# Kernel optimization log

Hardware: AMD Instinct MI355X
Metric: run time of the kernel (lower is better)

## Reference

```python
import jax, jax.numpy as jnp
import numpy as np

B, C, N, T = 16, 32, 400, 12
R, G, E, H = 64, 16, 64, 2
DH = E // H
FE = 4 * E
N1 = N2 = N3 = N4 = 0.5


def layernorm(x, w, b, eps=1e-5):
    m = x.mean(-1, keepdims=True)
    v = x.var(-1, keepdims=True)
    return (x - m) / jnp.sqrt(v + eps) * w + b


def asym_adj(A):
    rowsum = A.sum(1)
    d_inv = jnp.where(rowsum > 0, 1.0 / rowsum, 0.0)
    return d_inv[:, None] * A


def gcn(x, supports, W, b):
    # CHGCNGCN with order=1: concat [x, x@a for a in supports] on channel dim, 1x1 conv
    outs = [x] + [jnp.einsum('bcvt,vw->bcwt', x, a) for a in supports]
    h = jnp.concatenate(outs, axis=1)
    return jnp.einsum('oc,bcvt->bovt', W, h) + b[None, :, None, None]


def setup_inputs() -> dict:
    key0 = jax.random.key(0)
    ks = jax.random.split(key0, 40)
    rn = lambda i, sh, s=1.0: jax.random.normal(ks[i], sh, dtype=jnp.float32) * s
    ru = lambda i, sh, s=1.0: jax.random.uniform(ks[i], sh, dtype=jnp.float32) * s
    inp = {
        'value': rn(0, (B, C, N, T)),
        'key': rn(1, (B, C, N, T)),
        'query': rn(2, (B, C, N, T)),
        'supports0': ru(3, (N, N), 1.0 / N),
        'supports1': ru(4, (N, N), 1.0 / N),
        'supports_r0': ru(5, (R, R), 1.0 / R),
        'supports_r1': ru(6, (R, R), 1.0 / R),
        'Mrg': ru(7, (R, G), 1.0 / R),
        'Mor': ru(8, (N, R), 1.0 / N),
        'D_S': ru(9, (N, N)),
        'W_conv1': rn(10, (E, C), (1.0 / C) ** 0.5),
        'b_conv1': jnp.zeros((E,), jnp.float32),
        'W_conv11': rn(11, (C, E), (1.0 / E) ** 0.5),
        'b_conv11': jnp.zeros((C,), jnp.float32),
        'W_gcn': rn(12, (C, 3 * C), (1.0 / (3 * C)) ** 0.5),
        'b_gcn': jnp.zeros((C,), jnp.float32),
        'W_embed': rn(13, (E, N), (1.0 / N) ** 0.5),
        'b_embed': jnp.zeros((E,), jnp.float32),
        'Wq': rn(14, (DH, DH), (1.0 / DH) ** 0.5),
        'Wk': rn(15, (DH, DH), (1.0 / DH) ** 0.5),
        'Wv': rn(16, (DH, DH), (1.0 / DH) ** 0.5),
        'W_fc': rn(17, (E, E), (1.0 / E) ** 0.5),
        'b_fc': jnp.zeros((E,), jnp.float32),
        'ln1_w': jnp.ones((E,), jnp.float32),
        'ln1_b': jnp.zeros((E,), jnp.float32),
        'ln2_w': jnp.ones((E,), jnp.float32),
        'ln2_b': jnp.zeros((E,), jnp.float32),
        'W_ff1': rn(18, (FE, E), (1.0 / E) ** 0.5),
        'b_ff1': jnp.zeros((FE,), jnp.float32),
        'W_ff2': rn(19, (E, FE), (1.0 / FE) ** 0.5),
        'b_ff2': jnp.zeros((E,), jnp.float32),
        'W_fs': rn(20, (E, E), (1.0 / E) ** 0.5),
        'b_fs': jnp.zeros((E,), jnp.float32),
        'W_fg': rn(21, (E, E), (1.0 / E) ** 0.5),
        'b_fg': jnp.zeros((E,), jnp.float32),
    }
    return inp


def _chgcn(x, supports, supports_r, Mrg, Mor, W_gcn, b_gcn):
    ho = gcn(x, supports, W_gcn, b_gcn)
    x_r = jnp.einsum('nr,bcnt->bcrt', Mor, x)            # Mor.T @ x
    hr = gcn(x_r, supports_r, W_gcn, b_gcn)
    xs = jnp.einsum('rg,bcrt->bcgt', Mrg, x_r)           # Mrg.T @ (Mor.T @ x)
    # data-dependent global adjacency (detached in torch -> stop_gradient)
    xg_mat = jnp.transpose(xs, (2, 1, 0, 3)).reshape(G, -1)   # (G, C*B*T)
    xgt_mat = jnp.transpose(xs, (3, 0, 1, 2)).reshape(-1, G)  # (T*B*C, G)
    Ag = jax.lax.stop_gradient(jax.nn.relu(xg_mat @ xgt_mat - 0.5))
    sg = [jax.nn.softmax(asym_adj(Ag), axis=-1),
          jax.nn.softmax(asym_adj(Ag.T), axis=-1)]
    xg = gcn(xs, sg, W_gcn, b_gcn)
    hr = hr + N1 * jax.nn.relu(jnp.einsum('rg,bcgt->bcrt', Mrg, xg))
    ho = ho + N2 * jax.nn.relu(jnp.einsum('nr,bcrt->bcnt', Mor, hr))
    hr = hr + N3 * jax.nn.relu(jnp.einsum('nr,bcnt->bcrt', Mor, ho))
    xg = xg + N4 * jax.nn.relu(jnp.einsum('rg,bcrt->bcgt', Mrg, hr))
    return ho, hr, xg


def _attention(q, Wq, Wk, Wv, W_fc, b_fc):
    # q: (B, N, T, E); value=key=query in STransformer.forward
    qh = q.reshape(B, N, T, H, DH)
    qq = jnp.einsum('bnthd,ed->bnthe', qh, Wq)
    kk = jnp.einsum('bnthd,ed->bnthe', qh, Wk)
    vv = jnp.einsum('bnthd,ed->bnthe', qh, Wv)
    energy = jnp.einsum('bqthd,bkthd->bqkth', qq, kk)
    attn = jax.nn.softmax(energy / (E ** 0.5), axis=2)
    out = jnp.einsum('bqkth,bkthd->bqthd', attn, vv).reshape(B, N, T, E)
    return jnp.einsum('bnte,oe->bnto', out, W_fc) + b_fc


def reference(value, key, query, supports0, supports1, supports_r0, supports_r1,
              Mrg, Mor, D_S, W_conv1, b_conv1, W_conv11, b_conv11, W_gcn, b_gcn,
              W_embed, b_embed, Wq, Wk, Wv, W_fc, b_fc, ln1_w, ln1_b, ln2_w,
              ln2_b, W_ff1, b_ff1, W_ff2, b_ff2, W_fs, b_fs, W_fg, b_fg):
    supports = [supports0, supports1]
    supports_r = [supports_r0, supports_r1]
    ho, xc, xs = _chgcn(query, supports, supports_r, Mrg, Mor, W_gcn, b_gcn)
    conv1 = lambda x: jnp.einsum('oc,bcnt->bont', W_conv1, x) + b_conv1[None, :, None, None]
    Xc = jnp.transpose(conv1(ho), (0, 2, 3, 1))        # (B, N, T, E)
    q = jnp.transpose(conv1(query), (0, 2, 3, 1))      # (B, N, T, E); value=key=q
    ds = jnp.einsum('nm,em->ne', D_S, W_embed) + b_embed   # (N, E)
    q = q + ds[None, :, None, :]
    attn = _attention(q, Wq, Wk, Wv, W_fc, b_fc)
    x = layernorm(attn + q, ln1_w, ln1_b)
    ff = jnp.einsum('bnte,oe->bnto', jax.nn.relu(
        jnp.einsum('bnte,fe->bntf', x, W_ff1) + b_ff1), W_ff2) + b_ff2
    U_S = layernorm(ff + x, ln2_w, ln2_b)
    g = jax.nn.sigmoid(jnp.einsum('bnte,oe->bnto', U_S, W_fs) + b_fs +
                       jnp.einsum('bnte,oe->bnto', Xc, W_fg) + b_fg)
    out = g * U_S + (1.0 - g) * Xc
    out = jnp.transpose(out, (0, 3, 1, 2))             # (B, E, N, T)
    out = jnp.einsum('oe,bent->bont', W_conv11, out) + b_conv11[None, :, None, None]
    return out, xc, xs
```

## Files before the change

### kernel.cpp

```cpp
#include <hip/hip_runtime.h>

#define TT 12

__global__ void __launch_bounds__(256) k_spatial(
    const float* __restrict__ M, int orientT, int Vin, int Vout,
    const float* __restrict__ in, const float* __restrict__ base,
    float scale, int do_relu, float* __restrict__ out)
{
    __shared__ float in_lds[400 * TT];
    int bc = blockIdx.x;
    const float* ib = in + (size_t)bc * Vin * TT;
    for (int i = threadIdx.x; i < Vin * TT; i += 256) in_lds[i] = ib[i];
    __syncthreads();
    int chunk = Vout / gridDim.y;
    int vo0 = blockIdx.y * chunk;
    size_t obase = (size_t)bc * Vout * TT;
    for (int idx = threadIdx.x; idx < chunk * TT; idx += 256) {
        int vo = vo0 + idx / TT, t = idx - (idx / TT) * TT;
        float acc = 0.f;
        if (orientT) {
            for (int vi = 0; vi < Vin; ++vi)
                acc += M[(size_t)vi * Vout + vo] * in_lds[vi * TT + t];
        } else {
            const float* Mr = M + (size_t)vo * Vin;
            for (int vi = 0; vi < Vin; ++vi)
                acc += Mr[vi] * in_lds[vi * TT + t];
        }
        if (do_relu) acc = fmaxf(acc, 0.f);
        acc *= scale;
        size_t oi = obase + (size_t)vo * TT + t;
        if (base) acc += base[oi];
        out[oi] = acc;
    }
}

__global__ void __launch_bounds__(256) k_gcn_combine(
    const float* __restrict__ x, const float* __restrict__ t0in,
    const float* __restrict__ t1in, const float* __restrict__ W,
    const float* __restrict__ bias, int V, float* __restrict__ out)
{
    __shared__ float xs_[96 * 33], t0s[96 * 33], t1s[96 * 33], WT[96 * 32];
    int nb = V / 8;
    int b = blockIdx.x / nb, n0 = (blockIdx.x % nb) * 8;
    for (int l = threadIdx.x; l < 96 * 32; l += 256) {
        int c3 = l >> 5, o = l & 31;
        WT[l] = W[o * 96 + c3];
    }
    for (int l = threadIdx.x; l < 3072; l += 256) {
        int c = l / 96, s = l - c * 96;
        size_t g = ((size_t)((b * 32 + c) * V) + n0 + s / 12) * 12 + (s % 12);
        xs_[s * 33 + c] = x[g];
        t0s[s * 33 + c] = t0in[g];
        t1s[s * 33 + c] = t1in[g];
    }
    __syncthreads();
    for (int idx = threadIdx.x; idx < 3072; idx += 256) {
        int o = idx / 96, s = idx - o * 96;
        float acc = bias[o];
        for (int c = 0; c < 32; ++c) {
            float a = xs_[s * 33 + c] * WT[c * 32 + o];
            float b2 = t0s[s * 33 + c] * WT[(32 + c) * 32 + o];
            float c2 = t1s[s * 33 + c] * WT[(64 + c) * 32 + o];
            acc += a + b2 + c2;
        }
        out[((size_t)(b * 32 + o) * V + n0) * 12 + s] = acc;
    }
}

__global__ void __launch_bounds__(256) k_conv1(
    const float* __restrict__ x, const float* __restrict__ W,
    const float* __restrict__ bias, const float* __restrict__ dsadd,
    float* __restrict__ out)
{
    __shared__ float xs_[96 * 33];
    __shared__ float WT[2048];
    int b = blockIdx.x / 50, n0 = (blockIdx.x % 50) * 8;
    for (int l = threadIdx.x; l < 2048; l += 256) {
        int c = l >> 6, o = l & 63;
        WT[l] = W[o * 32 + c];
    }
    for (int l = threadIdx.x; l < 3072; l += 256) {
        int c = l / 96, s = l - c * 96;
        xs_[s * 33 + c] = x[((size_t)(b * 32 + c) * 400 + n0 + s / 12) * 12 + (s % 12)];
    }
    __syncthreads();
    for (int idx = threadIdx.x; idx < 6144; idx += 256) {
        int s = idx >> 6, o = idx & 63;
        float acc = bias[o];
        for (int c = 0; c < 32; ++c) acc += xs_[s * 33 + c] * WT[(c << 6) + o];
        if (dsadd) acc += dsadd[(n0 + s / 12) * 64 + o];
        out[((size_t)b * 4800 + n0 * 12 + s) * 64 + o] = acc;
    }
}

__global__ void __launch_bounds__(64) k_ds(
    const float* __restrict__ D_S, const float* __restrict__ Wem,
    const float* __restrict__ bem, float* __restrict__ ds)
{
    __shared__ float row[400];
    int n = blockIdx.x;
    for (int i = threadIdx.x; i < 400; i += 64) row[i] = D_S[n * 400 + i];
    __syncthreads();
    int e = threadIdx.x;
    float acc = bem[e];
    const float* we = Wem + (size_t)e * 400;
    for (int m = 0; m < 400; ++m) acc += row[m] * we[m];
    ds[n * 64 + e] = acc;
}

__global__ void __launch_bounds__(256) k_agp(const float* __restrict__ xs,
                                             float* __restrict__ Ag)
{
    __shared__ float A[256 * 17], Bv[256 * 17];
    int i = blockIdx.x * 256 + threadIdx.x;
    int c1 = i / 192, b1 = (i / 12) & 15, t1 = i % 12;
    int t2 = i >> 9, b2 = (i >> 5) & 15, c2 = i & 31;
    for (int g = 0; g < 16; ++g) {
        A[threadIdx.x * 17 + g] = xs[((size_t)(b1 * 32 + c1) * 16 + g) * 12 + t1];
        Bv[threadIdx.x * 17 + g] = xs[((size_t)(b2 * 32 + c2) * 16 + g) * 12 + t2];
    }
    __syncthreads();
    int g1 = threadIdx.x >> 4, g2 = threadIdx.x & 15;
    float acc = 0.f;
    for (int k = 0; k < 256; ++k) acc += A[k * 17 + g1] * Bv[k * 17 + g2];
    atomicAdd(&Ag[threadIdx.x], acc);
}

__global__ void __launch_bounds__(64) k_agf(const float* __restrict__ Ag,
                                            float* __restrict__ sg0,
                                            float* __restrict__ sg1)
{
    __shared__ float Ar[256], rs[16], cs[16];
    int tid = threadIdx.x;
    for (int l = tid; l < 256; l += 64) Ar[l] = fmaxf(Ag[l] - 0.5f, 0.f);
    __syncthreads();
    if (tid < 16) {
        float r = 0.f, c = 0.f;
        for (int j = 0; j < 16; ++j) { r += Ar[tid * 16 + j]; c += Ar[j * 16 + tid]; }
        rs[tid] = (r > 0.f) ? 1.f / r : 0.f;
        cs[tid] = (c > 0.f) ? 1.f / c : 0.f;
    }
    __syncthreads();
    if (tid < 16) {
        float v[16], m, s;
        m = -1e30f;
        for (int j = 0; j < 16; ++j) { v[j] = Ar[tid * 16 + j] * rs[tid]; m = fmaxf(m, v[j]); }
        s = 0.f;
        for (int j = 0; j < 16; ++j) { v[j] = expf(v[j] - m); s += v[j]; }
        for (int j = 0; j < 16; ++j) sg0[tid * 16 + j] = v[j] / s;
        m = -1e30f;
        for (int j = 0; j < 16; ++j) { v[j] = Ar[j * 16 + tid] * cs[tid]; m = fmaxf(m, v[j]); }
        s = 0.f;
        for (int j = 0; j < 16; ++j) { v[j] = expf(v[j] - m); s += v[j]; }
        for (int j = 0; j < 16; ++j) sg1[tid * 16 + j] = v[j] / s;
    }
}

__global__ void __launch_bounds__(256) k_qkv(
    const float* __restrict__ q, const float* __restrict__ Wq,
    const float* __restrict__ Wk, const float* __restrict__ Wv,
    float* __restrict__ qq, float* __restrict__ kk, float* __restrict__ vv)
{
    __shared__ float qs[64 * 33], wqT[1024], wkT[1024], wvT[1024];
    int g = blockIdx.x, n0 = blockIdx.y * 64;
    int b = g / 24, rem = g % 24, t = rem >> 1, h = rem & 1;
    int tid = threadIdx.x;
    for (int i = tid; i < 1024; i += 256) {
        int dd = i >> 5, e = i & 31;
        wqT[i] = Wq[e * 32 + dd];
        wkT[i] = Wk[e * 32 + dd];
        wvT[i] = Wv[e * 32 + dd];
    }
    for (int i = tid; i < 2048; i += 256) {
        int n = i >> 5, dd = i & 31;
        int gn = n0 + n;
        qs[n * 33 + dd] = (gn < 400)
            ? q[((size_t)b * 4800 + gn * 12 + t) * 64 + h * 32 + dd] : 0.f;
    }
    __syncthreads();
    int e = tid & 31, ng = tid >> 5;
    float aq[8], ak[8], av[8];
    #pragma unroll
    for (int k = 0; k < 8; ++k) { aq[k] = 0.f; ak[k] = 0.f; av[k] = 0.f; }
    for (int dd = 0; dd < 32; ++dd) {
        float wq = wqT[dd * 32 + e], wk = wkT[dd * 32 + e], wv = wvT[dd * 32 + e];
        #pragma unroll
        for (int k = 0; k < 8; ++k) {
            float xv = qs[(ng + 8 * k) * 33 + dd];
            aq[k] += xv * wq; ak[k] += xv * wk; av[k] += xv * wv;
        }
    }
    #pragma unroll
    for (int k = 0; k < 8; ++k) {
        int gn = n0 + ng + 8 * k;
        if (gn < 400) {
            size_t a = ((size_t)g * 400 + gn) * 32 + e;
            qq[a] = aq[k]; kk[a] = ak[k]; vv[a] = av[k];
        }
    }
}

__global__ void __launch_bounds__(1024, 4) k_attn3(
    const float* __restrict__ qq, const float* __restrict__ kk,
    const float* __restrict__ vv, float* __restrict__ attnO)
{
    extern __shared__ float lds[];
    float* kkT = lds;
    float* vvs = kkT + 14368;
    float* pbuf = vvs + 12800;

    int g = blockIdx.x >> 1, rh = blockIdx.x & 1;
    const float* qq_g = qq + (size_t)g * 12800;
    const float* kk_g = kk + (size_t)g * 12800;
    const float* vv_g = vv + (size_t)g * 12800;
    int tid = threadIdx.x;

    for (int i = tid; i < 1568; i += 1024) {
        int d = i / 49, c = i - d * 49;
        kkT[d * 449 + 400 + c] = 0.f;
    }
    for (int i = tid; i < 12800; i += 1024) {
        int k = i >> 5, d = i & 31;
        kkT[d * 449 + k] = kk_g[i];
        vvs[i] = vv_g[i];
    }
    __syncthreads();

    int w = tid >> 6, l = tid & 63;
    float* pw = pbuf + w * 800;
    int b = g / 24, rem = g % 24, t = rem >> 1, h = rem & 1;
    size_t obase = ((size_t)b * 4800 + t) * 64 + h * 32;

    for (int r0 = rh * 200 + w * 2; r0 < rh * 200 + 200; r0 += 32) {
        float e0[7], e1[7];
        #pragma unroll
        for (int j = 0; j < 7; ++j) { e0[j] = 0.f; e1[j] = 0.f; }

        for (int db = 0; db < 4; ++db) {
            float q0[8], q1[8];
            #pragma unroll
            for (int dd = 0; dd < 8; ++dd) {
                q0[dd] = qq_g[(r0 + 0) * 32 + db * 8 + dd];
                q1[dd] = qq_g[(r0 + 1) * 32 + db * 8 + dd];
            }
            #pragma unroll
            for (int j = 0; j < 7; ++j) {
                #pragma unroll
                for (int dd = 0; dd < 8; ++dd) {
                    float kv = kkT[(db * 8 + dd) * 449 + j * 64 + l];
                    e0[j] += q0[dd] * kv;
                    e1[j] += q1[dd] * kv;
                }
            }
        }
        bool ok6 = (l < 16);
        float s0v, s1v;
        {
            if (!ok6) e0[6] = -1e30f;
            float m = e0[0];
            #pragma unroll
            for (int j = 1; j < 7; ++j) m = fmaxf(m, e0[j]);
            #pragma unroll
            for (int off = 32; off; off >>= 1) m = fmaxf(m, __shfl_xor(m, off));
            float ss = 0.f;
            #pragma unroll
            for (int j = 0; j < 7; ++j) {
                e0[j] = __expf((e0[j] - m) * 0.125f);
                ss += e0[j];
            }
            #pragma unroll
            for (int off = 32; off; off >>= 1) ss += __shfl_xor(ss, off);
            s0v = ss;
            #pragma unroll
            for (int j = 0; j < 6; ++j) pw[j * 64 + l] = e0[j];
            if (ok6) pw[384 + l] = e0[6];
        }
        {
            if (!ok6) e1[6] = -1e30f;
            float m = e1[0];
            #pragma unroll
            for (int j = 1; j < 7; ++j) m = fmaxf(m, e1[j]);
            #pragma unroll
            for (int off = 32; off; off >>= 1) m = fmaxf(m, __shfl_xor(m, off));
            float ss = 0.f;
            #pragma unroll
            for (int j = 0; j < 7; ++j) {
                e1[j] = __expf((e1[j] - m) * 0.125f);
                ss += e1[j];
            }
            #pragma unroll
            for (int off = 32; off; off >>= 1) ss += __shfl_xor(ss, off);
            s1v = ss;
            #pragma unroll
            for (int j = 0; j < 6; ++j) pw[400 + j * 64 + l] = e1[j];
            if (ok6) pw[784 + l] = e1[6];
        }
        asm volatile("" ::: "memory");

        int hh = l >> 5, d = l & 31;
        float o0 = 0.f, o1 = 0.f;
        const float* pr0 = pw + hh * 200;
        const float* pr1 = pw + 400 + hh * 200;
        int kb0 = hh * 200;
        for (int kb = 0; kb < 200; kb += 4) {
            float4 p0 = *(const float4*)(pr0 + kb);
            float4 p1 = *(const float4*)(pr1 + kb);
            int k = kb0 + kb;
            float v0 = vvs[(k + 0) * 32 + d];
            float v1 = vvs[(k + 1) * 32 + d];
            float v2 = vvs[(k + 2) * 32 + d];
            float v3 = vvs[(k + 3) * 32 + d];
            o0 += p0.x * v0 + p0.y * v1 + p0.z * v2 + p0.w * v3;
            o1 += p1.x * v0 + p1.y * v1 + p1.z * v2 + p1.w * v3;
        }
        asm volatile("" ::: "memory");
        o0 += __shfl_down(o0, 32);
        o1 += __shfl_down(o1, 32);
        if (l < 32) {
            attnO[obase + (size_t)(r0 + 0) * 768 + d] = o0 / s0v;
            attnO[obase + (size_t)(r0 + 1) * 768 + d] = o1 / s1v;
        }
    }
}

__global__ void __launch_bounds__(256) k_A1n(
    const float* __restrict__ attnO, const float* __restrict__ Wfc,
    const float* __restrict__ bfc, const float* __restrict__ qbuf,
    const float* __restrict__ w1, const float* __restrict__ b1,
    float* __restrict__ xout)
{
    __shared__ float WT[64 * 65], ao[64 * 65], qs[64 * 65];
    size_t R0 = (size_t)blockIdx.x * 64;
    int tid = threadIdx.x;
    for (int l = tid; l < 4096; l += 256) {
        int o = l >> 6, e = l & 63;
        WT[e * 65 + o] = Wfc[l];
    }
    for (int i = tid; i < 1024; i += 256) {
        int r = i >> 4, c4 = (i & 15) * 4;
        *(float4*)(ao + r * 65 + c4) = *(const float4*)(attnO + (R0 + r) * 64 + c4);
        *(float4*)(qs + r * 65 + c4) = *(const float4*)(qbuf + (R0 + r) * 64 + c4);
    }
    __syncthreads();

    int oj = tid & 15, ri = tid >> 4;
    float acc[4][4];
    #pragma unroll
    for (int rr = 0; rr < 4; ++rr)
        #pragma unroll
        for (int cc = 0; cc < 4; ++cc) acc[rr][cc] = 0.f;

    for (int eb = 0; eb < 16; ++eb) {
        float w[4][4], u[4][4];
        #pragma unroll
        for (int k = 0; k < 4; ++k) {
            float4 t = *(const float4*)(WT + (eb * 4 + k) * 65 + 4 * oj);
            w[k][0] = t.x; w[k][1] = t.y; w[k][2] = t.z; w[k][3] = t.w;
        }
        #pragma unroll
        for (int rr = 0; rr < 4; ++rr) {
            float4 t = *(const float4*)(ao + (4 * ri + rr) * 65 + eb * 4);
            u[rr][0] = t.x; u[rr][1] = t.y; u[rr][2] = t.z; u[rr][3] = t.w;
        }
        #pragma unroll
        for (int rr = 0; rr < 4; ++rr)
            #pragma unroll
            for (int k = 0; k < 4; ++k) {
                float uv = u[rr][k];
                acc[rr][0] += uv * w[k][0];
                acc[rr][1] += uv * w[k][1];
                acc[rr][2] += uv * w[k][2];
                acc[rr][3] += uv * w[k][3];
            }
    }
    float bf[4];
    #pragma unroll
    for (int cc = 0; cc < 4; ++cc) bf[cc] = bfc[4 * oj + cc];
    #pragma unroll
    for (int rr = 0; rr < 4; ++rr)
        #pragma unroll
        for (int cc = 0; cc < 4; ++cc) {
            int r = 4 * ri + rr, o = 4 * oj + cc;
            qs[r * 65 + o] += acc[rr][cc] + bf[cc];
        }
    __syncthreads();
    int r = tid >> 2, sb = tid & 3;
    float vals[16];
    float sm = 0.f;
    #pragma unroll
    for (int i = 0; i < 4; ++i) {
        float4 t = *(const float4*)(qs + r * 65 + sb * 16 + 4 * i);
        vals[4 * i + 0] = t.x; vals[4 * i + 1] = t.y;
        vals[4 * i + 2] = t.z; vals[4 * i + 3] = t.w;
        sm += t.x + t.y + t.z + t.w;
    }
    sm += __shfl_xor(sm, 1); sm += __shfl_xor(sm, 2);
    float mean = sm * (1.f / 64.f);
    float vs = 0.f;
    #pragma unroll
    for (int i = 0; i < 16; ++i) { float dv = vals[i] - mean; vs += dv * dv; }
    vs += __shfl_xor(vs, 1); vs += __shfl_xor(vs, 2);
    float inv = rsqrtf(vs * (1.f / 64.f) + 1e-5f);
    #pragma unroll
    for (int i = 0; i < 16; ++i) {
        int o = sb * 16 + i;
        xout[(R0 + r) * 64 + o] = (vals[i] - mean) * inv * w1[o] + b1[o];
    }
}

__global__ void __launch_bounds__(512, 2) k_A2n(
    const float* __restrict__ xin, const float* __restrict__ Wff1,
    const float* __restrict__ bff1, const float* __restrict__ Wff2,
    const float* __restrict__ bff2, const float* __restrict__ w2,
    const float* __restrict__ b2, float* __restrict__ US)
{
    extern __shared__ float lds[];
    float* xs = lds;
    float* Wb = xs + 4160;
    float* fhT = Wb + 16384;
    size_t R0 = (size_t)blockIdx.x * 64;
    int tid = threadIdx.x;
    for (int i = tid; i < 4096; i += 512) {
        int r = i >> 6, e = i & 63;
        xs[r * 65 + e] = xin[(R0 + r) * 64 + e];
    }
    for (int i = tid; i < 16384; i += 512) {
        int e = i >> 8, f = i & 255;
        Wb[i] = Wff1[f * 64 + e];
    }
    __syncthreads();
    int l = tid & 63, g = tid >> 6;
    {
        float acc[4][8];
        #pragma unroll
        for (int j = 0; j < 4; ++j)
            #pragma unroll
            for (int ri = 0; ri < 8; ++ri) acc[j][ri] = 0.f;
        for (int e = 0; e < 64; ++e) {
            float xr[8];
            #pragma unroll
            for (int ri = 0; ri < 8; ++ri) xr[ri] = xs[(g * 8 + ri) * 65 + e];
            #pragma unroll
            for (int j = 0; j < 4; ++j) {
                float wv = Wb[e * 256 + l + 64 * j];
                #pragma unroll
                for (int ri = 0; ri < 8; ++ri) acc[j][ri] += xr[ri] * wv;
            }
        }
        #pragma unroll
        for (int j = 0; j < 4; ++j) {
            float bb = bff1[l + 64 * j];
            #pragma unroll
            for (int ri = 0; ri < 8; ++ri)
                fhT[(l + 64 * j) * 65 + g * 8 + ri] = fmaxf(acc[j][ri] + bb, 0.f);
        }
    }
    __syncthreads();
    for (int i = tid; i < 16384; i += 512) {
        int f = i >> 6, o = i & 63;
        Wb[i] = Wff2[o * 256 + f];
    }
    __syncthreads();
    float acc2[8];
    #pragma unroll
    for (int oi = 0; oi < 8; ++oi) acc2[oi] = 0.f;
    for (int f = 0; f < 256; ++f) {
        float fv = fhT[f * 65 + l];
        float4 wa = *(const float4*)(Wb + f * 64 + g * 8);
        float4 wb_ = *(const float4*)(Wb + f * 64 + g * 8 + 4);
        acc2[0] += fv * wa.x;  acc2[1] += fv * wa.y;
        acc2[2] += fv * wa.z;  acc2[3] += fv * wa.w;
        acc2[4] += fv * wb_.x; acc2[5] += fv * wb_.y;
        acc2[6] += fv * wb_.z; acc2[7] += fv * wb_.w;
    }
    __syncthreads();
    float* lnb = Wb;
    float* mM = Wb + 4160;
    float* mI = Wb + 4224;
    #pragma unroll
    for (int oi = 0; oi < 8; ++oi) {
        int o = g * 8 + oi;
        lnb[l * 65 + o] = acc2[oi] + bff2[o] + xs[l * 65 + o];
    }
    __syncthreads();
    int r = tid >> 3, sb = tid & 7;
    float v[8];
    float sm = 0.f;
    #pragma unroll
    for (int i = 0; i < 8; ++i) { v[i] = lnb[r * 65 + sb + 8 * i]; sm += v[i]; }
    sm += __shfl_xor(sm, 1); sm += __shfl_xor(sm, 2); sm += __shfl_xor(sm, 4);
    float mean = sm * (1.f / 64.f);
    float vs = 0.f;
    #pragma unroll
    for (int i = 0; i < 8; ++i) { float dv = v[i] - mean; vs += dv * dv; }
    vs += __shfl_xor(vs, 1); vs += __shfl_xor(vs, 2); vs += __shfl_xor(vs, 4);
    float inv = rsqrtf(vs * (1.f / 64.f) + 1e-5f);
    if (sb == 0) { mM[r] = mean; mI[r] = inv; }
    __syncthreads();
    for (int i = tid; i < 4096; i += 512) {
        int rr = i >> 6, o = i & 63;
        US[(R0 + rr) * 64 + o] = (lnb[rr * 65 + o] - mM[rr]) * mI[rr] * w2[o] + b2[o];
    }
}

__global__ void __launch_bounds__(256) k_A3n(
    const float* __restrict__ US, const float* __restrict__ Xc,
    const float* __restrict__ Wfs, const float* __restrict__ bfs,
    const float* __restrict__ Wfg, const float* __restrict__ bfg,
    const float* __restrict__ Wc11, const float* __restrict__ bc11,
    float* __restrict__ out)
{
    extern __shared__ float lds[];
    float* WsT = lds;
    float* WgT = WsT + 4160;
    float* WcT = WgT + 4160;
    float* us  = WcT + 2112;
    float* xc  = us + 4160;
    size_t R0 = (size_t)blockIdx.x * 64;
    int tid = threadIdx.x;
    for (int l = tid; l < 4096; l += 256) {
        int o = l >> 6, e = l & 63;
        WsT[e * 65 + o] = Wfs[l];
        WgT[e * 65 + o] = Wfg[l];
    }
    for (int l = tid; l < 2048; l += 256) {
        int oc = l >> 6, e = l & 63;
        WcT[e * 33 + oc] = Wc11[l];
    }
    for (int i = tid; i < 1024; i += 256) {
        int r = i >> 4, c4 = (i & 15) * 4;
        *(float4*)(us + r * 65 + c4) = *(const float4*)(US + (R0 + r) * 64 + c4);
        *(float4*)(xc + r * 65 + c4) = *(const float4*)(Xc + (R0 + r) * 64 + c4);
    }
    __syncthreads();

    int oj = tid & 15, ri = tid >> 4;
    float a1[4][4], a2[4][4];
    #pragma unroll
    for (int rr = 0; rr < 4; ++rr)
        #pragma unroll
        for (int cc = 0; cc < 4; ++cc) { a1[rr][cc] = 0.f; a2[rr][cc] = 0.f; }

    for (int eb = 0; eb < 16; ++eb) {
        {
            float w[4][4], u[4][4];
            #pragma unroll
            for (int k = 0; k < 4; ++k) {
                float4 t = *(const float4*)(WsT + (eb * 4 + k) * 65 + 4 * oj);
                w[k][0] = t.x; w[k][1] = t.y; w[k][2] = t.z; w[k][3] = t.w;
            }
            #pragma unroll
            for (int rr = 0; rr < 4; ++rr) {
                float4 t = *(const float4*)(us + (4 * ri + rr) * 65 + eb * 4);
                u[rr][0] = t.x; u[rr][1] = t.y; u[rr][2] = t.z; u[rr][3] = t.w;
            }
            #pragma unroll
            for (int rr = 0; rr < 4; ++rr)
                #pragma unroll
                for (int k = 0; k < 4; ++k) {
                    float uv = u[rr][k];
                    a1[rr][0] += uv * w[k][0];
                    a1[rr][1] += uv * w[k][1];
                    a1[rr][2] += uv * w[k][2];
                    a1[rr][3] += uv * w[k][3];
                }
        }
        {
            float w[4][4], u[4][4];
            #pragma unroll
            for (int k = 0; k < 4; ++k) {
                float4 t = *(const float4*)(WgT + (eb * 4 + k) * 65 + 4 * oj);
                w[k][0] = t.x; w[k][1] = t.y; w[k][2] = t.z; w[k][3] = t.w;
            }
            #pragma unroll
            for (int rr = 0; rr < 4; ++rr) {
                float4 t = *(const float4*)(xc + (4 * ri + rr) * 65 + eb * 4);
                u[rr][0] = t.x; u[rr][1] = t.y; u[rr][2] = t.z; u[rr][3] = t.w;
            }
            #pragma unroll
            for (int rr = 0; rr < 4; ++rr)
                #pragma unroll
                for (int k = 0; k < 4; ++k) {
                    float uv = u[rr][k];
                    a2[rr][0] += uv * w[k][0];
                    a2[rr][1] += uv * w[k][1];
                    a2[rr][2] += uv * w[k][2];
                    a2[rr][3] += uv * w[k][3];
                }
        }
    }
    __syncthreads();
    float bs[4], bg2[4];
    #pragma unroll
    for (int cc = 0; cc < 4; ++cc) { bs[cc] = bfs[4 * oj + cc]; bg2[cc] = bfg[4 * oj + cc]; }
    #pragma unroll
    for (int rr = 0; rr < 4; ++rr)
        #pragma unroll
        for (int cc = 0; cc < 4; ++cc) {
            int r = 4 * ri + rr, o = 4 * oj + cc;
            float gg = 1.f / (1.f + __expf(-(a1[rr][cc] + bs[cc] + a2[rr][cc] + bg2[cc])));
            float uv = us[r * 65 + o], xv = xc[r * 65 + o];
            us[r * 65 + o] = gg * uv + (1.f - gg) * xv;
        }
    __syncthreads();

    int ocj = tid & 7, rg = tid >> 3;
    float c2[2][4];
    #pragma unroll
    for (int rr = 0; rr < 2; ++rr)
        #pragma unroll
        for (int cc = 0; cc < 4; ++cc) c2[rr][cc] = bc11[4 * ocj + cc];
    for (int eb = 0; eb < 16; ++eb) {
        float w[4][4], p[2][4];
        #pragma unroll
        for (int k = 0; k < 4; ++k) {
            float4 t = *(const float4*)(WcT + (eb * 4 + k) * 33 + 4 * ocj);
            w[k][0] = t.x; w[k][1] = t.y; w[k][2] = t.z; w[k][3] = t.w;
        }
        #pragma unroll
        for (int rr = 0; rr < 2; ++rr) {
            float4 t = *(const float4*)(us + (2 * rg + rr) * 65 + eb * 4);
            p[rr][0] = t.x; p[rr][1] = t.y; p[rr][2] = t.z; p[rr][3] = t.w;
        }
        #pragma unroll
        for (int rr = 0; rr < 2; ++rr)
            #pragma unroll
            for (int k = 0; k < 4; ++k) {
                float pv = p[rr][k];
                c2[rr][0] += pv * w[k][0];
                c2[rr][1] += pv * w[k][1];
                c2[rr][2] += pv * w[k][2];
                c2[rr][3] += pv * w[k][3];
            }
    }
    int b = (int)(R0 / 4800);
    int rr0 = (int)(R0 % 4800);
    #pragma unroll
    for (int cc = 0; cc < 4; ++cc)
        #pragma unroll
        for (int rr = 0; rr < 2; ++rr)
            out[(size_t)(b * 32 + 4 * ocj + cc) * 4800 + rr0 + 2 * rg + rr] = c2[rr][cc];
}

extern "C" void kernel_launch(void* const* d_in, const int* in_sizes, int n_in,
                              void* d_out, int out_size, void* d_ws, size_t ws_size,
                              hipStream_t stream)
{
    (void)in_sizes; (void)n_in; (void)out_size; (void)ws_size;
    const float* query = (const float*)d_in[2];
    const float* s0    = (const float*)d_in[3];
    const float* s1    = (const float*)d_in[4];
    const float* sr0   = (const float*)d_in[5];
    const float* sr1   = (const float*)d_in[6];
    const float* Mrg   = (const float*)d_in[7];
    const float* Mor   = (const float*)d_in[8];
    const float* D_S   = (const float*)d_in[9];
    const float* Wc1   = (const float*)d_in[10];
    const float* bc1   = (const float*)d_in[11];
    const float* Wc11  = (const float*)d_in[12];
    const float* bc11  = (const float*)d_in[13];
    const float* Wg    = (const float*)d_in[14];
    const float* bg    = (const float*)d_in[15];
    const float* Wem   = (const float*)d_in[16];
    const float* bem   = (const float*)d_in[17];
    const float* Wq    = (const float*)d_in[18];
    const float* Wk    = (const float*)d_in[19];
    const float* Wv    = (const float*)d_in[20];
    const float* Wfc   = (const float*)d_in[21];
    const float* bfc   = (const float*)d_in[22];
    const float* ln1w  = (const float*)d_in[23];
    const float* ln1b  = (const float*)d_in[24];
    const float* ln2w  = (const float*)d_in[25];
    const float* ln2b  = (const float*)d_in[26];
    const float* Wff1  = (const float*)d_in[27];
    const float* bff1  = (const float*)d_in[28];
    const float* Wff2  = (const float*)d_in[29];
    const float* bff2  = (const float*)d_in[30];
    const float* Wfs   = (const float*)d_in[31];
    const float* bfs   = (const float*)d_in[32];
    const float* Wfg   = (const float*)d_in[33];
    const float* bfg   = (const float*)d_in[34];

    float* ws = (float*)d_ws;
    size_t off = 0;
    auto alloc = [&](size_t n) { float* p = ws + off; off += n; return p; };
    float* q_buf = alloc(4915200);
    float* Xc    = alloc(4915200);
    float* x_buf = alloc(4915200);
    float* US    = alloc(4915200);
    float* ho    = alloc(2457600);
    float* t0    = alloc(2457600);
    float* t1    = alloc(2457600);
    float* xr    = alloc(393216);
    float* tr0   = alloc(393216);
    float* tr1   = alloc(393216);
    float* hr    = alloc(393216);
    float* xsg   = alloc(98304);
    float* tg0   = alloc(98304);
    float* tg1   = alloc(98304);
    float* xg0   = alloc(98304);
    float* dsb   = alloc(25600);
    float* Ag    = alloc(256);
    float* sg0   = alloc(256);
    float* sg1   = alloc(256);

    float* qq    = Xc;
    float* kk    = t0;
    float* vv    = US;
    float* attnO = x_buf;

    float* out_main = (float*)d_out;
    float* out_xc   = out_main + 2457600;
    float* out_xs   = out_main + 2850816;

    hipFuncSetAttribute((const void*)k_attn3,
                        hipFuncAttributeMaxDynamicSharedMemorySize, 159872);
    hipFuncSetAttribute((const void*)k_A2n,
                        hipFuncAttributeMaxDynamicSharedMemorySize, 148736);
    hipFuncSetAttribute((const void*)k_A3n,
                        hipFuncAttributeMaxDynamicSharedMemorySize, 75008);

    hipMemsetAsync(Ag, 0, 256 * sizeof(float), stream);

    k_ds<<<400, 64, 0, stream>>>(D_S, Wem, bem, dsb);
    k_conv1<<<800, 256, 0, stream>>>(query, Wc1, bc1, dsb, q_buf);
    k_qkv<<<dim3(384, 7), 256, 0, stream>>>(q_buf, Wq, Wk, Wv, qq, kk, vv);
    k_attn3<<<768, 1024, 159872, stream>>>(qq, kk, vv, attnO);
    k_A1n<<<1200, 256, 0, stream>>>(attnO, Wfc, bfc, q_buf, ln1w, ln1b, x_buf);
    k_A2n<<<1200, 512, 148736, stream>>>(x_buf, Wff1, bff1, Wff2, bff2,
                                         ln2w, ln2b, US);

    k_spatial<<<dim3(512, 4), 256, 0, stream>>>(s0, 1, 400, 400, query, nullptr, 1.f, 0, t0);
    k_spatial<<<dim3(512, 4), 256, 0, stream>>>(s1, 1, 400, 400, query, nullptr, 1.f, 0, t1);
    k_gcn_combine<<<800, 256, 0, stream>>>(query, t0, t1, Wg, bg, 400, ho);
    k_spatial<<<dim3(512, 1), 256, 0, stream>>>(Mor, 1, 400, 64, query, nullptr, 1.f, 0, xr);
    k_spatial<<<dim3(512, 1), 256, 0, stream>>>(sr0, 1, 64, 64, xr, nullptr, 1.f, 0, tr0);
    k_spatial<<<dim3(512, 1), 256, 0, stream>>>(sr1, 1, 64, 64, xr, nullptr, 1.f, 0, tr1);
    k_gcn_combine<<<128, 256, 0, stream>>>(xr, tr0, tr1, Wg, bg, 64, hr);
    k_spatial<<<dim3(512, 1), 256, 0, stream>>>(Mrg, 1, 64, 16, xr, nullptr, 1.f, 0, xsg);
    k_agp<<<24, 256, 0, stream>>>(xsg, Ag);
    k_agf<<<1, 64, 0, stream>>>(Ag, sg0, sg1);
    k_spatial<<<dim3(512, 1), 256, 0, stream>>>(sg0, 1, 16, 16, xsg, nullptr, 1.f, 0, tg0);
    k_spatial<<<dim3(512, 1), 256, 0, stream>>>(sg1, 1, 16, 16, xsg, nullptr, 1.f, 0, tg1);
    k_gcn_combine<<<32, 256, 0, stream>>>(xsg, tg0, tg1, Wg, bg, 16, xg0);
    k_spatial<<<dim3(512, 1), 256, 0, stream>>>(Mrg, 0, 16, 64, xg0, hr, 0.5f, 1, hr);
    k_spatial<<<dim3(512, 4), 256, 0, stream>>>(Mor, 0, 64, 400, hr, ho, 0.5f, 1, ho);
    k_spatial<<<dim3(512, 1), 256, 0, stream>>>(Mor, 1, 400, 64, ho, hr, 0.5f, 1, out_xc);
    k_spatial<<<dim3(512, 1), 256, 0, stream>>>(Mrg, 1, 64, 16, out_xc, xg0, 0.5f, 1, out_xs);

    k_conv1<<<800, 256, 0, stream>>>(ho, Wc1, bc1, nullptr, Xc);
    k_A3n<<<1200, 256, 75008, stream>>>(US, Xc, Wfs, bfs, Wfg, bfg, Wc11, bc11, out_main);
}
```

Before: 1.434 ms.

## Register-block spatial, gcn-combine, conv1 and attention kernels with vectorized tiles

The transposed-orientation spatial matmul now computes a 4x4 register tile per thread using float4 loads of M and of the LDS input, and stores float4 outputs. The gcn_combine and conv1 kernels switch to a channel-major LDS layout, so each thread computes 4 consecutive time slots from float4 reads. The attention kernel processes 4 query rows per wave instead of 2, which halves K reads per row, and stores V transposed so the PV product reads contiguous float2 values. The cost targeted is LDS and global load traffic per FMA, in exchange for higher register pressure and slightly more LDS.

```diff
diff --git a/kernel.cpp b/kernel.cpp
--- a/kernel.cpp
+++ b/kernel.cpp
@@ -15,22 +15,55 @@
     int chunk = Vout / gridDim.y;
     int vo0 = blockIdx.y * chunk;
     size_t obase = (size_t)bc * Vout * TT;
-    for (int idx = threadIdx.x; idx < chunk * TT; idx += 256) {
-        int vo = vo0 + idx / TT, t = idx - (idx / TT) * TT;
-        float acc = 0.f;
-        if (orientT) {
-            for (int vi = 0; vi < Vin; ++vi)
-                acc += M[(size_t)vi * Vout + vo] * in_lds[vi * TT + t];
-        } else {
+    if (orientT) {
+        int ng = chunk >> 2;
+        for (int idx = threadIdx.x; idx < ng * 3; idx += 256) {
+            int vgi = idx / 3, tj = idx - (idx / 3) * 3;
+            int vo = vo0 + vgi * 4;
+            float a0x=0,a0y=0,a0z=0,a0w=0, a1x=0,a1y=0,a1z=0,a1w=0;
+            float a2x=0,a2y=0,a2z=0,a2w=0, a3x=0,a3y=0,a3z=0,a3w=0;
+            for (int vi = 0; vi < Vin; ++vi) {
+                float4 m = *(const float4*)(M + (size_t)vi * Vout + vo);
+                float4 xv = *(const float4*)(in_lds + vi * 12 + tj * 4);
+                a0x += m.x*xv.x; a0y += m.x*xv.y; a0z += m.x*xv.z; a0w += m.x*xv.w;
+                a1x += m.y*xv.x; a1y += m.y*xv.y; a1z += m.y*xv.z; a1w += m.y*xv.w;
+                a2x += m.z*xv.x; a2y += m.z*xv.y; a2z += m.z*xv.z; a2w += m.z*xv.w;
+                a3x += m.w*xv.x; a3y += m.w*xv.y; a3z += m.w*xv.z; a3w += m.w*xv.w;
+            }
+            float4 r[4];
+            r[0] = make_float4(a0x,a0y,a0z,a0w);
+            r[1] = make_float4(a1x,a1y,a1z,a1w);
+            r[2] = make_float4(a2x,a2y,a2z,a2w);
+            r[3] = make_float4(a3x,a3y,a3z,a3w);
+            #pragma unroll
+            for (int c = 0; c < 4; ++c) {
+                float4 v = r[c];
+                if (do_relu) {
+                    v.x = fmaxf(v.x, 0.f); v.y = fmaxf(v.y, 0.f);
+                    v.z = fmaxf(v.z, 0.f); v.w = fmaxf(v.w, 0.f);
+                }
+                v.x *= scale; v.y *= scale; v.z *= scale; v.w *= scale;
+                size_t oi = obase + (size_t)(vo + c) * 12 + tj * 4;
+                if (base) {
+                    float4 bb = *(const float4*)(base + oi);
+                    v.x += bb.x; v.y += bb.y; v.z += bb.z; v.w += bb.w;
+                }
+                *(float4*)(out + oi) = v;
+            }
+        }
+    } else {
+        for (int idx = threadIdx.x; idx < chunk * TT; idx += 256) {
+            int vo = vo0 + idx / TT, t = idx - (idx / TT) * TT;
+            float acc = 0.f;
             const float* Mr = M + (size_t)vo * Vin;
             for (int vi = 0; vi < Vin; ++vi)
                 acc += Mr[vi] * in_lds[vi * TT + t];
-        }
-        if (do_relu) acc = fmaxf(acc, 0.f);
-        acc *= scale;
-        size_t oi = obase + (size_t)vo * TT + t;
-        if (base) acc += base[oi];
-        out[oi] = acc;
+            if (do_relu) acc = fmaxf(acc, 0.f);
+            acc *= scale;
+            size_t oi = obase + (size_t)vo * TT + t;
+            if (base) acc += base[oi];
+            out[oi] = acc;
+        }
     }
 }
 
@@ -39,31 +72,39 @@
     const float* __restrict__ t1in, const float* __restrict__ W,
     const float* __restrict__ bias, int V, float* __restrict__ out)
 {
-    __shared__ float xs_[96 * 33], t0s[96 * 33], t1s[96 * 33], WT[96 * 32];
+    __shared__ float xsc[32 * 100], t0c[32 * 100], t1c[32 * 100], WT[96 * 32];
     int nb = V / 8;
     int b = blockIdx.x / nb, n0 = (blockIdx.x % nb) * 8;
-    for (int l = threadIdx.x; l < 96 * 32; l += 256) {
+    for (int l = threadIdx.x; l < 3072; l += 256) {
         int c3 = l >> 5, o = l & 31;
         WT[l] = W[o * 96 + c3];
     }
     for (int l = threadIdx.x; l < 3072; l += 256) {
         int c = l / 96, s = l - c * 96;
-        size_t g = ((size_t)((b * 32 + c) * V) + n0 + s / 12) * 12 + (s % 12);
-        xs_[s * 33 + c] = x[g];
-        t0s[s * 33 + c] = t0in[g];
-        t1s[s * 33 + c] = t1in[g];
-    }
-    __syncthreads();
-    for (int idx = threadIdx.x; idx < 3072; idx += 256) {
-        int o = idx / 96, s = idx - o * 96;
-        float acc = bias[o];
+        size_t g = (size_t)(b * 32 + c) * V * 12 + n0 * 12 + s;
+        xsc[c * 100 + s] = x[g];
+        t0c[c * 100 + s] = t0in[g];
+        t1c[c * 100 + s] = t1in[g];
+    }
+    __syncthreads();
+    int o = threadIdx.x & 31, slot = threadIdx.x >> 5;
+    for (int sg = slot; sg < 24; sg += 8) {
+        float bz = bias[o];
+        float c0 = bz, c1 = bz, c2 = bz, c3v = bz;
         for (int c = 0; c < 32; ++c) {
-            float a = xs_[s * 33 + c] * WT[c * 32 + o];
-            float b2 = t0s[s * 33 + c] * WT[(32 + c) * 32 + o];
-            float c2 = t1s[s * 33 + c] * WT[(64 + c) * 32 + o];
-            acc += a + b2 + c2;
-        }
-        out[((size_t)(b * 32 + o) * V + n0) * 12 + s] = acc;
+            float w0 = WT[c * 32 + o];
+            float w1 = WT[(32 + c) * 32 + o];
+            float w2 = WT[(64 + c) * 32 + o];
+            float4 xv = *(const float4*)(xsc + c * 100 + 4 * sg);
+            float4 y0 = *(const float4*)(t0c + c * 100 + 4 * sg);
+            float4 y1 = *(const float4*)(t1c + c * 100 + 4 * sg);
+            c0 += xv.x * w0 + y0.x * w1 + y1.x * w2;
+            c1 += xv.y * w0 + y0.y * w1 + y1.y * w2;
+            c2 += xv.z * w0 + y0.z * w1 + y1.z * w2;
+            c3v += xv.w * w0 + y0.w * w1 + y1.w * w2;
+        }
+        size_t ob = ((size_t)(b * 32 + o) * V + n0) * 12 + 4 * sg;
+        *(float4*)(out + ob) = make_float4(c0, c1, c2, c3v);
     }
 }
 
@@ -72,7 +113,7 @@
     const float* __restrict__ bias, const float* __restrict__ dsadd,
     float* __restrict__ out)
 {
-    __shared__ float xs_[96 * 33];
+    __shared__ float xsc[32 * 100];
     __shared__ float WT[2048];
     int b = blockIdx.x / 50, n0 = (blockIdx.x % 50) * 8;
     for (int l = threadIdx.x; l < 2048; l += 256) {
@@ -81,15 +122,24 @@
     }
     for (int l = threadIdx.x; l < 3072; l += 256) {
         int c = l / 96, s = l - c * 96;
-        xs_[s * 33 + c] = x[((size_t)(b * 32 + c) * 400 + n0 + s / 12) * 12 + (s % 12)];
-    }
-    __syncthreads();
-    for (int idx = threadIdx.x; idx < 6144; idx += 256) {
-        int s = idx >> 6, o = idx & 63;
-        float acc = bias[o];
-        for (int c = 0; c < 32; ++c) acc += xs_[s * 33 + c] * WT[(c << 6) + o];
-        if (dsadd) acc += dsadd[(n0 + s / 12) * 64 + o];
-        out[((size_t)b * 4800 + n0 * 12 + s) * 64 + o] = acc;
+        xsc[c * 100 + s] = x[(size_t)(b * 32 + c) * 4800 + n0 * 12 + s];
+    }
+    __syncthreads();
+    int o = threadIdx.x & 63, slot = threadIdx.x >> 6;
+    for (int sg = slot; sg < 24; sg += 4) {
+        float ad = bias[o];
+        if (dsadd) ad += dsadd[(n0 + (4 * sg) / 12) * 64 + o];
+        float c0 = ad, c1 = ad, c2 = ad, c3v = ad;
+        for (int c = 0; c < 32; ++c) {
+            float w = WT[(c << 6) + o];
+            float4 xv = *(const float4*)(xsc + c * 100 + 4 * sg);
+            c0 += xv.x * w; c1 += xv.y * w; c2 += xv.z * w; c3v += xv.w * w;
+        }
+        size_t ob = ((size_t)b * 4800 + n0 * 12 + 4 * sg) * 64 + o;
+        out[ob] = c0;
+        out[ob + 64] = c1;
+        out[ob + 128] = c2;
+        out[ob + 192] = c3v;
     }
 }
 
@@ -200,14 +250,30 @@
     }
 }
 
-__global__ void __launch_bounds__(1024, 4) k_attn3(
+#define SMAX_ROW(EARR, PROW, SVAR) {                                          \
+    if (l >= 16) EARR[6] = -1e30f;                                            \
+    float m_ = EARR[0];                                                       \
+    _Pragma("unroll") for (int j_ = 1; j_ < 7; ++j_) m_ = fmaxf(m_, EARR[j_]);\
+    _Pragma("unroll") for (int o_ = 32; o_; o_ >>= 1)                         \
+        m_ = fmaxf(m_, __shfl_xor(m_, o_));                                   \
+    float ss_ = 0.f;                                                          \
+    _Pragma("unroll") for (int j_ = 0; j_ < 7; ++j_) {                        \
+        EARR[j_] = __expf((EARR[j_] - m_) * 0.125f); ss_ += EARR[j_]; }       \
+    _Pragma("unroll") for (int o_ = 32; o_; o_ >>= 1)                         \
+        ss_ += __shfl_xor(ss_, o_);                                           \
+    SVAR = ss_;                                                               \
+    _Pragma("unroll") for (int j_ = 0; j_ < 6; ++j_)                          \
+        (PROW)[j_ * 64 + l] = EARR[j_];                                       \
+    if (l < 16) (PROW)[384 + l] = EARR[6]; }
+
+__global__ void __launch_bounds__(1024, 4) k_attn4(
     const float* __restrict__ qq, const float* __restrict__ kk,
     const float* __restrict__ vv, float* __restrict__ attnO)
 {
     extern __shared__ float lds[];
     float* kkT = lds;
-    float* vvs = kkT + 14368;
-    float* pbuf = vvs + 12800;
+    float* vvT = kkT + 14368;
+    float* pbuf = vvT + 12864;
 
     int g = blockIdx.x >> 1, rh = blockIdx.x & 1;
     const float* qq_g = qq + (size_t)g * 12800;
@@ -222,7 +288,7 @@
     for (int i = tid; i < 12800; i += 1024) {
         int k = i >> 5, d = i & 31;
         kkT[d * 449 + k] = kk_g[i];
-        vvs[i] = vv_g[i];
+        vvT[d * 402 + k] = vv_g[i];
     }
     __syncthreads();
 
@@ -230,18 +296,22 @@
     float* pw = pbuf + w * 800;
     int b = g / 24, rem = g % 24, t = rem >> 1, h = rem & 1;
     size_t obase = ((size_t)b * 4800 + t) * 64 + h * 32;
-
-    for (int r0 = rh * 200 + w * 2; r0 < rh * 200 + 200; r0 += 32) {
-        float e0[7], e1[7];
-        #pragma unroll
-        for (int j = 0; j < 7; ++j) { e0[j] = 0.f; e1[j] = 0.f; }
+    int hh = l >> 5, d = l & 31;
+    int kb0 = hh * 200;
+
+    for (int r0 = rh * 200 + w * 4; r0 < rh * 200 + 200; r0 += 64) {
+        float e0[7], e1[7], e2[7], e3[7];
+        #pragma unroll
+        for (int j = 0; j < 7; ++j) { e0[j]=0.f; e1[j]=0.f; e2[j]=0.f; e3[j]=0.f; }
 
         for (int db = 0; db < 4; ++db) {
-            float q0[8], q1[8];
+            float q0[8], q1[8], q2[8], q3[8];
             #pragma unroll
             for (int dd = 0; dd < 8; ++dd) {
                 q0[dd] = qq_g[(r0 + 0) * 32 + db * 8 + dd];
                 q1[dd] = qq_g[(r0 + 1) * 32 + db * 8 + dd];
+                q2[dd] = qq_g[(r0 + 2) * 32 + db * 8 + dd];
+                q3[dd] = qq_g[(r0 + 3) * 32 + db * 8 + dd];
             }
             #pragma unroll
             for (int j = 0; j < 7; ++j) {
@@ -250,76 +320,62 @@
                     float kv = kkT[(db * 8 + dd) * 449 + j * 64 + l];
                     e0[j] += q0[dd] * kv;
                     e1[j] += q1[dd] * kv;
+                    e2[j] += q2[dd] * kv;
+                    e3[j] += q3[dd] * kv;
                 }
             }
         }
-        bool ok6 = (l < 16);
-        float s0v, s1v;
+        float s0v, s1v, s2v, s3v;
+        SMAX_ROW(e0, pw, s0v);
+        SMAX_ROW(e1, pw + 400, s1v);
+        asm volatile("" ::: "memory");
         {
-            if (!ok6) e0[6] = -1e30f;
-            float m = e0[0];
-            #pragma unroll
-            for (int j = 1; j < 7; ++j) m = fmaxf(m, e0[j]);
-            #pragma unroll
-            for (int off = 32; off; off >>= 1) m = fmaxf(m, __shfl_xor(m, off));
-            float ss = 0.f;
-            #pragma unroll
-            for (int j = 0; j < 7; ++j) {
-                e0[j] = __expf((e0[j] - m) * 0.125f);
-                ss += e0[j];
-            }
-            #pragma unroll
-            for (int off = 32; off; off >>= 1) ss += __shfl_xor(ss, off);
-            s0v = ss;
-            #pragma unroll
-            for (int j = 0; j < 6; ++j) pw[j * 64 + l] = e0[j];
-            if (ok6) pw[384 + l] = e0[6];
-        }
+            float o0 = 0.f, o1 = 0.f;
+            const float* pr0 = pw + hh * 200;
+            const float* pr1 = pw + 400 + hh * 200;
+            const float* vr = vvT + d * 402 + kb0;
+            for (int kb = 0; kb < 200; kb += 4) {
+                float4 p0 = *(const float4*)(pr0 + kb);
+                float4 p1 = *(const float4*)(pr1 + kb);
+                float2 va = *(const float2*)(vr + kb);
+                float2 vb = *(const float2*)(vr + kb + 2);
+                o0 += p0.x * va.x + p0.y * va.y + p0.z * vb.x + p0.w * vb.y;
+                o1 += p1.x * va.x + p1.y * va.y + p1.z * vb.x + p1.w * vb.y;
+            }
+            asm volatile("" ::: "memory");
+            o0 += __shfl_down(o0, 32);
+            o1 += __shfl_down(o1, 32);
+            if (l < 32) {
+                attnO[obase + (size_t)(r0 + 0) * 768 + d] = o0 / s0v;
+                attnO[obase + (size_t)(r0 + 1) * 768 + d] = o1 / s1v;
+            }
+        }
+        asm volatile("" ::: "memory");
+        SMAX_ROW(e2, pw, s2v);
+        SMAX_ROW(e3, pw + 400, s3v);
+        asm volatile("" ::: "memory");
         {
-            if (!ok6) e1[6] = -1e30f;
-            float m = e1[0];
-            #pragma unroll
-            for (int j = 1; j < 7; ++j) m = fmaxf(m, e1[j]);
-            #pragma unroll
-            for (int off = 32; off; off >>= 1) m = fmaxf(m, __shfl_xor(m, off));
-            float ss = 0.f;
-            #pragma unroll
-            for (int j = 0; j < 7; ++j) {
-                e1[j] = __expf((e1[j] - m) * 0.125f);
-                ss += e1[j];
-            }
-            #pragma unroll
-            for (int off = 32; off; off >>= 1) ss += __shfl_xor(ss, off);
-            s1v = ss;
-            #pragma unroll
-            for (int j = 0; j < 6; ++j) pw[400 + j * 64 + l] = e1[j];
-            if (ok6) pw[784 + l] = e1[6];
+            float o2 = 0.f, o3 = 0.f;
+            const float* pr0 = pw + hh * 200;
+            const float* pr1 = pw + 400 + hh * 200;
+            const float* vr = vvT + d * 402 + kb0;
+            for (int kb = 0; kb < 200; kb += 4) {
+                float4 p0 = *(const float4*)(pr0 + kb);
+                float4 p1 = *(const float4*)(pr1 + kb);
+                float2 va = *(const float2*)(vr + kb);
+                float2 vb = *(const float2*)(vr + kb + 2);
+                o2 += p0.x * va.x + p0.y * va.y + p0.z * vb.x + p0.w * vb.y;
+                o3 += p1.x * va.x + p1.y * va.y + p1.z * vb.x + p1.w * vb.y;
+            }
+            asm volatile("" ::: "memory");
+            o2 += __shfl_down(o2, 32);
+            o3 += __shfl_down(o3, 32);
+            if (l < 32) {
+                attnO[obase + (size_t)(r0 + 2) * 768 + d] = o2 / s2v;
+                attnO[obase + (size_t)(r0 + 3) * 768 + d] = o3 / s3v;
+            }
         }
         asm volatile("" ::: "memory");
-
-        int hh = l >> 5, d = l & 31;
-        float o0 = 0.f, o1 = 0.f;
-        const float* pr0 = pw + hh * 200;
-        const float* pr1 = pw + 400 + hh * 200;
-        int kb0 = hh * 200;
-        for (int kb = 0; kb < 200; kb += 4) {
-            float4 p0 = *(const float4*)(pr0 + kb);
-            float4 p1 = *(const float4*)(pr1 + kb);
-            int k = kb0 + kb;
-            float v0 = vvs[(k + 0) * 32 + d];
-            float v1 = vvs[(k + 1) * 32 + d];
-            float v2 = vvs[(k + 2) * 32 + d];
-            float v3 = vvs[(k + 3) * 32 + d];
-            o0 += p0.x * v0 + p0.y * v1 + p0.z * v2 + p0.w * v3;
-            o1 += p1.x * v0 + p1.y * v1 + p1.z * v2 + p1.w * v3;
-        }
-        asm volatile("" ::: "memory");
-        o0 += __shfl_down(o0, 32);
-        o1 += __shfl_down(o1, 32);
-        if (l < 32) {
-            attnO[obase + (size_t)(r0 + 0) * 768 + d] = o0 / s0v;
-            attnO[obase + (size_t)(r0 + 1) * 768 + d] = o1 / s1v;
-        }
     }
 }
 
@@ -713,8 +769,8 @@
     float* out_xc   = out_main + 2457600;
     float* out_xs   = out_main + 2850816;
 
-    hipFuncSetAttribute((const void*)k_attn3,
-                        hipFuncAttributeMaxDynamicSharedMemorySize, 159872);
+    hipFuncSetAttribute((const void*)k_attn4,
+                        hipFuncAttributeMaxDynamicSharedMemorySize, 160128);
     hipFuncSetAttribute((const void*)k_A2n,
                         hipFuncAttributeMaxDynamicSharedMemorySize, 148736);
     hipFuncSetAttribute((const void*)k_A3n,
@@ -725,7 +781,7 @@
     k_ds<<<400, 64, 0, stream>>>(D_S, Wem, bem, dsb);
     k_conv1<<<800, 256, 0, stream>>>(query, Wc1, bc1, dsb, q_buf);
     k_qkv<<<dim3(384, 7), 256, 0, stream>>>(q_buf, Wq, Wk, Wv, qq, kk, vv);
-    k_attn3<<<768, 1024, 159872, stream>>>(qq, kk, vv, attnO);
+    k_attn4<<<768, 1024, 160128, stream>>>(qq, kk, vv, attnO);
     k_A1n<<<1200, 256, 0, stream>>>(attnO, Wfc, bfc, q_buf, ln1w, ln1b, x_buf);
     k_A2n<<<1200, 512, 148736, stream>>>(x_buf, Wff1, bff1, Wff2, bff2,
                                          ln2w, ln2b, US);
```

Result: slower. 3.005 ms (+109.5%).
